# Kernel tuning notes

Measured on AMD Instinct MI355X. Metric: run time of the kernel, lower is better.

Reference implementation:

```python
import jax, jax.numpy as jnp
import numpy as np

N = 8192
PERCENT_ON = 0.1
K = int(round(N * PERCENT_ON))  # 819
BOOST_STRENGTH = 1.0


def setup_inputs() -> dict:
    key = jax.random.key(0)
    k1, k2 = jax.random.split(key)
    x = jax.random.normal(k1, (4096, N), dtype=jnp.float32)
    duty_cycles = jax.random.uniform(k2, (N,), dtype=jnp.float32) * 0.2
    return {"x": x, "duty_cycles": duty_cycles}


def reference(x, duty_cycles):
    # boost factors: exp((target_density - duty_cycle) * boost_strength)
    boost_strength = jnp.maximum(jnp.float32(BOOST_STRENGTH), 0.0)
    target_density = jnp.float32(K / N)
    boost_factors = jnp.exp((target_density - duty_cycles) * boost_strength)
    boosted = x * boost_factors  # [B, N]
    # top-k on boosted values, but transmit ORIGINAL x values at winning units
    _, idx = jax.lax.top_k(boosted, K)  # idx: [B, K]
    updates = jnp.take_along_axis(x, idx, axis=1)  # [B, K]
    rows = jnp.arange(x.shape[0])[:, None]  # [B, 1]
    out = jnp.zeros_like(x).at[rows, idx].set(updates)
    return out
```

## Files before the change

### kernel.cpp

```cpp
#include <hip/hip_runtime.h>
#include <math.h>

#define NCOL 8192
#define NROW 4096
#define KSEL 819
#define TPB  128
#define VPT  16
#define NBKT 1024
#define KPIV 0xBF866666u
#define LCAP 64

typedef float f32x4 __attribute__((ext_vector_type(4)));

__device__ __align__(16) float g_boost[NCOL];

__global__ void boost_kernel(const float* __restrict__ duty) {
    int i = blockIdx.x * blockDim.x + threadIdx.x;
    if (i < NCOL) {
        float diff = (0.0999755859375f - duty[i]);
        g_boost[i] = (float)exp((double)diff);
    }
}

__device__ __forceinline__ unsigned f2k(float f) {
    unsigned u = __float_as_uint(f);
    return u ^ (0x80000000u | (unsigned)((int)u >> 31));
}
__device__ __forceinline__ int kbucket(unsigned k) {
    int b = (int)(k >> 14) - (int)(KPIV >> 14);
    return (b > NBKT - 1) ? (NBKT - 1) : b;
}

__global__ __launch_bounds__(TPB) void kwinners_kernel(const float* __restrict__ x,
                                                       float* __restrict__ out) {
    __shared__ __align__(16) int hist[NBKT];
    __shared__ unsigned list[LCAP];
    __shared__ int wtot[2];
    __shared__ int lds_cnt, lds_sel, lds_R, lds_E;

    const int t = threadIdx.x, lane = t & 63, w = t >> 6;
    const int row = blockIdx.x;
    const f32x4* x4 = (const f32x4*)(x + (size_t)row * NCOL);
    const f32x4* b4 = (const f32x4*)g_boost;
    f32x4* o4 = (f32x4*)(out + (size_t)row * NCOL);

    unsigned kr[VPT][4];

    {
        const int4 z = make_int4(0, 0, 0, 0);
        ((int4*)hist)[2 * t] = z; ((int4*)hist)[2 * t + 1] = z;
        if (t == 0) lds_cnt = 0;
    }
#pragma unroll
    for (int j = 0; j < VPT; ++j) {
        f32x4 xx = x4[t + TPB * j];
        f32x4 bb = b4[t + TPB * j];
        kr[j][0] = f2k(xx.x * bb.x);
        kr[j][1] = f2k(xx.y * bb.y);
        kr[j][2] = f2k(xx.z * bb.z);
        kr[j][3] = f2k(xx.w * bb.w);
    }
    __syncthreads();

#pragma unroll
    for (int j = 0; j < VPT; ++j)
#pragma unroll
        for (int c = 0; c < 4; ++c) {
            unsigned k = kr[j][c];
            if (k > KPIV) atomicAdd(&hist[kbucket(k)], 1);
        }
    __syncthreads();

    int arr[16];
    {
        int4 a0 = ((const int4*)hist)[4 * lane + 0];
        int4 a1 = ((const int4*)hist)[4 * lane + 1];
        int4 a2 = ((const int4*)hist)[4 * lane + 2];
        int4 a3 = ((const int4*)hist)[4 * lane + 3];
        arr[0]=a0.x; arr[1]=a0.y; arr[2]=a0.z; arr[3]=a0.w;
        arr[4]=a1.x; arr[5]=a1.y; arr[6]=a1.z; arr[7]=a1.w;
        arr[8]=a2.x; arr[9]=a2.y; arr[10]=a2.z; arr[11]=a2.w;
        arr[12]=a3.x; arr[13]=a3.y; arr[14]=a3.z; arr[15]=a3.w;
    }
    int ts = 0;
#pragma unroll
    for (int b = 0; b < 16; ++b) ts += arr[b];
    int s = ts;
#pragma unroll
    for (int off = 1; off < 64; off <<= 1) {
        int o = __shfl_down(s, off);
        if (lane + off < 64) s += o;
    }
    const int C = __shfl(s, 0);

    unsigned th = 0; int Rf = 0, E = 0;
    bool fb = (C < KSEL);

    if (!fb) {
        const int S_ab = s - ts;
        bool cross = (S_ab < KSEL) && (S_ab + ts >= KSEL);
        int sel_l = 0, r1_l = 0;
        if (cross) {
            int cum = S_ab;
#pragma unroll
            for (int b = 15; b >= 0; --b) {
                int nx = cum + arr[b];
                if (cum < KSEL && nx >= KSEL) { sel_l = 16 * lane + b; r1_l = KSEL - cum; }
                cum = nx;
            }
        }
        unsigned long long m = __ballot(cross);
        int src = (int)__ffsll(m) - 1;
        const int sel = __shfl(sel_l, src);
        const int R1  = __shfl(r1_l, src);

#pragma unroll
        for (int j = 0; j < VPT; ++j)
#pragma unroll
            for (int c = 0; c < 4; ++c) {
                unsigned k = kr[j][c];
                if (k > KPIV && kbucket(k) == sel) {
                    int sl = atomicAdd(&lds_cnt, 1);
                    if (sl < LCAP) list[sl] = k;
                }
            }
        __syncthreads();
        const int n = lds_cnt;
        if (n > LCAP) fb = true;
        else {
            unsigned myk = (lane < n) ? list[lane] : 0u;
            int g = 0, e = 0;
            for (int i = 0; i < n; ++i) {
                unsigned ki = __shfl(myk, i);
                g += (ki > myk) ? 1 : 0;
                e += (ki == myk) ? 1 : 0;
            }
            unsigned cand = (lane < n && g < R1 && g + e >= R1) ? myk : 0u;
#pragma unroll
            for (int off = 1; off < 64; off <<= 1) {
                unsigned o = __shfl_xor(cand, off);
                cand = (o > cand) ? o : cand;
            }
            th = cand;

            int GE = 0;
#pragma unroll
            for (int j = 0; j < VPT; ++j) {
                f32x4 xx = x4[t + TPB * j];
                unsigned k0 = kr[j][0], k1 = kr[j][1], k2 = kr[j][2], k3 = kr[j][3];
                GE += (k0 > th) + (k1 > th) + (k2 > th) + (k3 > th);
                GE += ((k0 == th) + (k1 == th) + (k2 == th) + (k3 == th)) << 16;
                f32x4 rr;
                rr.x = (k0 >= th) ? xx.x : 0.0f;
                rr.y = (k1 >= th) ? xx.y : 0.0f;
                rr.z = (k2 >= th) ? xx.z : 0.0f;
                rr.w = (k3 >= th) ? xx.w : 0.0f;
                __builtin_nontemporal_store(rr, &o4[t + TPB * j]);
            }
#pragma unroll
            for (int off = 1; off < 64; off <<= 1) GE += __shfl_xor(GE, off);
            if (lane == 0) wtot[w] = GE;
            __syncthreads();
            const int GEt = wtot[0] + wtot[1];
            const int G = GEt & 0xFFFF, Eg = GEt >> 16;
            if (G < KSEL && G + Eg >= KSEL) { Rf = KSEL - G; E = Eg; }
            else fb = true;
        }
    }

    if (fb) {
        asm volatile("s_waitcnt vmcnt(0)" ::: "memory");
        __syncthreads();
        unsigned prefix = 0; int R = KSEL;
        for (int p = 0; p < 4; ++p) {
            const int sh = 24 - 8 * p;
            if (t < 64) ((int4*)hist)[t] = make_int4(0, 0, 0, 0);
            __syncthreads();
#pragma unroll
            for (int j = 0; j < VPT; ++j)
#pragma unroll
                for (int c = 0; c < 4; ++c) {
                    unsigned k = kr[j][c];
                    if (p == 0 || (k >> (sh + 8)) == (prefix >> (sh + 8)))
                        atomicAdd(&hist[(k >> sh) & 255u], 1);
                }
            __syncthreads();
            const int b0 = hist[2 * t], b1 = hist[2 * t + 1];
            int ts2 = b0 + b1, s2 = ts2;
#pragma unroll
            for (int off = 1; off < 64; off <<= 1) {
                int o = __shfl_down(s2, off);
                if (lane + off < 64) s2 += o;
            }
            if (lane == 0) wtot[w] = s2;
            __syncthreads();
            const int S_later = (w == 0) ? wtot[1] : 0;
            const int S_ab2 = (s2 - ts2) + S_later;
            if (S_ab2 < R && S_ab2 + ts2 >= R) {
                int cum = S_ab2;
                int nx = cum + b1;
                if (cum < R && nx >= R) { lds_sel = 2 * t + 1; lds_R = R - cum; lds_E = b1; }
                cum = nx; nx = cum + b0;
                if (cum < R && nx >= R) { lds_sel = 2 * t;     lds_R = R - cum; lds_E = b0; }
            }
            __syncthreads();
            prefix |= ((unsigned)lds_sel) << sh;
            R = lds_R;
        }
        th = prefix; Rf = R; E = lds_E;
#pragma unroll
        for (int j = 0; j < VPT; ++j) {
            f32x4 xx = x4[t + TPB * j];
            f32x4 rr;
            rr.x = (kr[j][0] >= th) ? xx.x : 0.0f;
            rr.y = (kr[j][1] >= th) ? xx.y : 0.0f;
            rr.z = (kr[j][2] >= th) ? xx.z : 0.0f;
            rr.w = (kr[j][3] >= th) ? xx.w : 0.0f;
            o4[t + TPB * j] = rr;
        }
    }

    if (E > Rf) {
        asm volatile("s_waitcnt vmcnt(0)" ::: "memory");
        __syncthreads();
        unsigned short* tl = (unsigned short*)hist;
        if (t == 0) lds_cnt = 0;
        __syncthreads();
#pragma unroll
        for (int j = 0; j < VPT; ++j)
#pragma unroll
            for (int c = 0; c < 4; ++c)
                if (kr[j][c] == th) {
                    int sl = atomicAdd(&lds_cnt, 1);
                    if (sl < 2048) tl[sl] = (unsigned short)(4 * (t + TPB * j) + c);
                }
        __syncthreads();
        const int ntie = lds_cnt;
        float* orow = out + (size_t)row * NCOL;
        if (ntie <= 2048) {
#pragma unroll
            for (int j = 0; j < VPT; ++j)
#pragma unroll
                for (int c = 0; c < 4; ++c)
                    if (kr[j][c] == th) {
                        const int col = 4 * (t + TPB * j) + c;
                        int rk = 0;
                        for (int i = 0; i < ntie; ++i) rk += (tl[i] < col) ? 1 : 0;
                        if (rk >= Rf) orow[col] = 0.0f;
                    }
        } else if (t == 0) {
            int seen = 0;
            for (int col = 0; col < NCOL; ++col) {
                float v = x[(size_t)row * NCOL + col] * g_boost[col];
                if (f2k(v) == th) { if (seen >= Rf) orow[col] = 0.0f; ++seen; }
            }
        }
    }
}

extern "C" void kernel_launch(void* const* d_in, const int* in_sizes, int n_in,
                              void* d_out, int out_size, void* d_ws, size_t ws_size,
                              hipStream_t stream) {
    const float* x = (const float*)d_in[0];
    const float* duty = (const float*)d_in[1];
    float* out = (float*)d_out;
    (void)in_sizes; (void)n_in; (void)out_size; (void)d_ws; (void)ws_size;

    boost_kernel<<<(NCOL + 255) / 256, 256, 0, stream>>>(duty);
    kwinners_kernel<<<NROW, TPB, 0, stream>>>(x, out);
}
```

Before: 73.59 us.

## Split k-winners into threshold and apply kernels with float-domain bucketing

Splits the fused kernel in two. The first kernel computes a per-row threshold, remainder and tie count and writes them to the workspace. A second kernel re-reads x and the boost factors, then writes the masked output. It also doubles threads per block, halves values per thread, and buckets on float values with a linear scale instead of key bits. The aim is to cut register pressure and raise occupancy, at the cost of reading x twice (an extra 128MB of traffic) plus an extra launch.

```diff
diff --git a/kernel.cpp b/kernel.cpp
--- a/kernel.cpp
+++ b/kernel.cpp
@@ -4,10 +4,11 @@
 #define NCOL 8192
 #define NROW 4096
 #define KSEL 819
-#define TPB  128
-#define VPT  16
+#define TPB  256
+#define VPT  8
 #define NBKT 1024
-#define KPIV 0xBF866666u
+#define PIV  1.05f
+#define BSCALE 512.0f
 #define LCAP 64
 
 typedef float f32x4 __attribute__((ext_vector_type(4)));
@@ -26,77 +27,83 @@
     unsigned u = __float_as_uint(f);
     return u ^ (0x80000000u | (unsigned)((int)u >> 31));
 }
-__device__ __forceinline__ int kbucket(unsigned k) {
-    int b = (int)(k >> 14) - (int)(KPIV >> 14);
+__device__ __forceinline__ float k2f(unsigned k) {
+    unsigned u = (k & 0x80000000u) ? (k ^ 0x80000000u) : ~k;
+    return __uint_as_float(u);
+}
+__device__ __forceinline__ int vbucket(float v) {
+    int b = (int)((v - PIV) * BSCALE);
+    b = (b < 0) ? 0 : b;
     return (b > NBKT - 1) ? (NBKT - 1) : b;
 }
 
-__global__ __launch_bounds__(TPB) void kwinners_kernel(const float* __restrict__ x,
-                                                       float* __restrict__ out) {
+__global__ __launch_bounds__(TPB) void thresh_kernel(const float* __restrict__ x,
+                                                     float* __restrict__ thf,
+                                                     int* __restrict__ rfo,
+                                                     int* __restrict__ eo) {
     __shared__ __align__(16) int hist[NBKT];
-    __shared__ unsigned list[LCAP];
-    __shared__ int wtot[2];
+    __shared__ float list[LCAP];
+    __shared__ int wtot[4];
     __shared__ int lds_cnt, lds_sel, lds_R, lds_E;
 
     const int t = threadIdx.x, lane = t & 63, w = t >> 6;
     const int row = blockIdx.x;
     const f32x4* x4 = (const f32x4*)(x + (size_t)row * NCOL);
     const f32x4* b4 = (const f32x4*)g_boost;
-    f32x4* o4 = (f32x4*)(out + (size_t)row * NCOL);
-
-    unsigned kr[VPT][4];
-
-    {
-        const int4 z = make_int4(0, 0, 0, 0);
-        ((int4*)hist)[2 * t] = z; ((int4*)hist)[2 * t + 1] = z;
-        if (t == 0) lds_cnt = 0;
-    }
+
+    f32x4 vv[VPT];
+
+    ((int4*)hist)[t] = make_int4(0, 0, 0, 0);
+    if (t == 0) lds_cnt = 0;
+
 #pragma unroll
     for (int j = 0; j < VPT; ++j) {
         f32x4 xx = x4[t + TPB * j];
         f32x4 bb = b4[t + TPB * j];
-        kr[j][0] = f2k(xx.x * bb.x);
-        kr[j][1] = f2k(xx.y * bb.y);
-        kr[j][2] = f2k(xx.z * bb.z);
-        kr[j][3] = f2k(xx.w * bb.w);
+        vv[j].x = xx.x * bb.x; vv[j].y = xx.y * bb.y;
+        vv[j].z = xx.z * bb.z; vv[j].w = xx.w * bb.w;
     }
     __syncthreads();
 
-#pragma unroll
-    for (int j = 0; j < VPT; ++j)
+    int cnt = 0;
+#pragma unroll
+    for (int j = 0; j < VPT; ++j) {
 #pragma unroll
         for (int c = 0; c < 4; ++c) {
-            unsigned k = kr[j][c];
-            if (k > KPIV) atomicAdd(&hist[kbucket(k)], 1);
-        }
+            float v = vv[j][c];
+            if (v > PIV) { ++cnt; atomicAdd(&hist[vbucket(v)], 1); }
+        }
+    }
+#pragma unroll
+    for (int off = 32; off; off >>= 1) cnt += __shfl_down(cnt, off);
+    if (lane == 0) wtot[w] = cnt;
     __syncthreads();
 
-    int arr[16];
-    {
-        int4 a0 = ((const int4*)hist)[4 * lane + 0];
-        int4 a1 = ((const int4*)hist)[4 * lane + 1];
-        int4 a2 = ((const int4*)hist)[4 * lane + 2];
-        int4 a3 = ((const int4*)hist)[4 * lane + 3];
-        arr[0]=a0.x; arr[1]=a0.y; arr[2]=a0.z; arr[3]=a0.w;
-        arr[4]=a1.x; arr[5]=a1.y; arr[6]=a1.z; arr[7]=a1.w;
-        arr[8]=a2.x; arr[9]=a2.y; arr[10]=a2.z; arr[11]=a2.w;
-        arr[12]=a3.x; arr[13]=a3.y; arr[14]=a3.z; arr[15]=a3.w;
-    }
-    int ts = 0;
-#pragma unroll
-    for (int b = 0; b < 16; ++b) ts += arr[b];
-    int s = ts;
-#pragma unroll
-    for (int off = 1; off < 64; off <<= 1) {
-        int o = __shfl_down(s, off);
-        if (lane + off < 64) s += o;
-    }
-    const int C = __shfl(s, 0);
-
-    unsigned th = 0; int Rf = 0, E = 0;
+    const int C = wtot[0] + wtot[1] + wtot[2] + wtot[3];
+    float th = 0.0f; int Rf = 0, E = 0;
     bool fb = (C < KSEL);
 
     if (!fb) {
+        int arr[16];
+        {
+            int4 a0 = ((const int4*)hist)[4 * lane + 0];
+            int4 a1 = ((const int4*)hist)[4 * lane + 1];
+            int4 a2 = ((const int4*)hist)[4 * lane + 2];
+            int4 a3 = ((const int4*)hist)[4 * lane + 3];
+            arr[0]=a0.x; arr[1]=a0.y; arr[2]=a0.z; arr[3]=a0.w;
+            arr[4]=a1.x; arr[5]=a1.y; arr[6]=a1.z; arr[7]=a1.w;
+            arr[8]=a2.x; arr[9]=a2.y; arr[10]=a2.z; arr[11]=a2.w;
+            arr[12]=a3.x; arr[13]=a3.y; arr[14]=a3.z; arr[15]=a3.w;
+        }
+        int ts = 0;
+#pragma unroll
+        for (int b = 0; b < 16; ++b) ts += arr[b];
+        int s = ts;
+#pragma unroll
+        for (int off = 1; off < 64; off <<= 1) {
+            int o = __shfl_down(s, off);
+            if (lane + off < 64) s += o;
+        }
         const int S_ab = s - ts;
         bool cross = (S_ab < KSEL) && (S_ab + ts >= KSEL);
         int sel_l = 0, r1_l = 0;
@@ -118,50 +125,42 @@
         for (int j = 0; j < VPT; ++j)
 #pragma unroll
             for (int c = 0; c < 4; ++c) {
-                unsigned k = kr[j][c];
-                if (k > KPIV && kbucket(k) == sel) {
+                float v = vv[j][c];
+                if (v > PIV && vbucket(v) == sel) {
                     int sl = atomicAdd(&lds_cnt, 1);
-                    if (sl < LCAP) list[sl] = k;
+                    if (sl < LCAP) list[sl] = v;
                 }
             }
         __syncthreads();
         const int n = lds_cnt;
-        if (n > LCAP) fb = true;
+        if (n > LCAP || n < 1) fb = true;
         else {
-            unsigned myk = (lane < n) ? list[lane] : 0u;
+            float myv = (lane < n) ? list[lane] : 0.0f;
             int g = 0, e = 0;
             for (int i = 0; i < n; ++i) {
-                unsigned ki = __shfl(myk, i);
-                g += (ki > myk) ? 1 : 0;
-                e += (ki == myk) ? 1 : 0;
-            }
-            unsigned cand = (lane < n && g < R1 && g + e >= R1) ? myk : 0u;
-#pragma unroll
-            for (int off = 1; off < 64; off <<= 1) {
-                unsigned o = __shfl_xor(cand, off);
-                cand = (o > cand) ? o : cand;
-            }
+                float vi = __shfl(myv, i);
+                g += (vi > myv) ? 1 : 0;
+                e += (vi == myv) ? 1 : 0;
+            }
+            float cand = (lane < n && g < R1 && g + e >= R1) ? myv : 0.0f;
+#pragma unroll
+            for (int off = 1; off < 64; off <<= 1)
+                cand = fmaxf(cand, __shfl_xor(cand, off));
             th = cand;
 
             int GE = 0;
 #pragma unroll
-            for (int j = 0; j < VPT; ++j) {
-                f32x4 xx = x4[t + TPB * j];
-                unsigned k0 = kr[j][0], k1 = kr[j][1], k2 = kr[j][2], k3 = kr[j][3];
-                GE += (k0 > th) + (k1 > th) + (k2 > th) + (k3 > th);
-                GE += ((k0 == th) + (k1 == th) + (k2 == th) + (k3 == th)) << 16;
-                f32x4 rr;
-                rr.x = (k0 >= th) ? xx.x : 0.0f;
-                rr.y = (k1 >= th) ? xx.y : 0.0f;
-                rr.z = (k2 >= th) ? xx.z : 0.0f;
-                rr.w = (k3 >= th) ? xx.w : 0.0f;
-                __builtin_nontemporal_store(rr, &o4[t + TPB * j]);
-            }
+            for (int j = 0; j < VPT; ++j)
+#pragma unroll
+                for (int c = 0; c < 4; ++c) {
+                    float v = vv[j][c];
+                    GE += (v > th ? 1 : 0) + (v == th ? (1 << 16) : 0);
+                }
 #pragma unroll
             for (int off = 1; off < 64; off <<= 1) GE += __shfl_xor(GE, off);
             if (lane == 0) wtot[w] = GE;
             __syncthreads();
-            const int GEt = wtot[0] + wtot[1];
+            const int GEt = wtot[0] + wtot[1] + wtot[2] + wtot[3];
             const int G = GEt & 0xFFFF, Eg = GEt >> 16;
             if (G < KSEL && G + Eg >= KSEL) { Rf = KSEL - G; E = Eg; }
             else fb = true;
@@ -169,24 +168,21 @@
     }
 
     if (fb) {
-        asm volatile("s_waitcnt vmcnt(0)" ::: "memory");
-        __syncthreads();
         unsigned prefix = 0; int R = KSEL;
         for (int p = 0; p < 4; ++p) {
             const int sh = 24 - 8 * p;
-            if (t < 64) ((int4*)hist)[t] = make_int4(0, 0, 0, 0);
+            hist[t] = 0;
             __syncthreads();
 #pragma unroll
             for (int j = 0; j < VPT; ++j)
 #pragma unroll
                 for (int c = 0; c < 4; ++c) {
-                    unsigned k = kr[j][c];
+                    unsigned k = f2k(vv[j][c]);
                     if (p == 0 || (k >> (sh + 8)) == (prefix >> (sh + 8)))
                         atomicAdd(&hist[(k >> sh) & 255u], 1);
                 }
             __syncthreads();
-            const int b0 = hist[2 * t], b1 = hist[2 * t + 1];
-            int ts2 = b0 + b1, s2 = ts2;
+            int h = hist[t], s2 = h;
 #pragma unroll
             for (int off = 1; off < 64; off <<= 1) {
                 int o = __shfl_down(s2, off);
@@ -194,65 +190,92 @@
             }
             if (lane == 0) wtot[w] = s2;
             __syncthreads();
-            const int S_later = (w == 0) ? wtot[1] : 0;
-            const int S_ab2 = (s2 - ts2) + S_later;
-            if (S_ab2 < R && S_ab2 + ts2 >= R) {
-                int cum = S_ab2;
-                int nx = cum + b1;
-                if (cum < R && nx >= R) { lds_sel = 2 * t + 1; lds_R = R - cum; lds_E = b1; }
-                cum = nx; nx = cum + b0;
-                if (cum < R && nx >= R) { lds_sel = 2 * t;     lds_R = R - cum; lds_E = b0; }
-            }
+            int S_later = 0;
+#pragma unroll
+            for (int w2 = 0; w2 < 4; ++w2) if (w2 > w) S_later += wtot[w2];
+            const int S_ab2 = (s2 - h) + S_later;
+            if (S_ab2 < R && S_ab2 + h >= R) { lds_sel = t; lds_R = R - S_ab2; lds_E = h; }
             __syncthreads();
             prefix |= ((unsigned)lds_sel) << sh;
             R = lds_R;
         }
-        th = prefix; Rf = R; E = lds_E;
+        th = k2f(prefix); Rf = R; E = lds_E;
+    }
+
+    if (t == 0) { thf[row] = th; rfo[row] = Rf; eo[row] = E; }
+}
+
+__global__ __launch_bounds__(TPB) void apply_kernel(const float* __restrict__ x,
+                                                    const float* __restrict__ thf,
+                                                    const int* __restrict__ rfo,
+                                                    const int* __restrict__ eo,
+                                                    float* __restrict__ out) {
+    __shared__ unsigned short tl[2048];
+    __shared__ int lds_cnt;
+
+    const int t = threadIdx.x;
+    const int row = blockIdx.x;
+    const f32x4* x4 = (const f32x4*)(x + (size_t)row * NCOL);
+    const f32x4* b4 = (const f32x4*)g_boost;
+    f32x4* o4 = (f32x4*)(out + (size_t)row * NCOL);
+
+    const float th = thf[row];
+    const int Rf = rfo[row], E = eo[row];
+
+#pragma unroll
+    for (int j = 0; j < VPT; ++j) {
+        f32x4 xx = x4[t + TPB * j];
+        f32x4 bb = b4[t + TPB * j];
+        f32x4 rr;
+        rr.x = (xx.x * bb.x >= th) ? xx.x : 0.0f;
+        rr.y = (xx.y * bb.y >= th) ? xx.y : 0.0f;
+        rr.z = (xx.z * bb.z >= th) ? xx.z : 0.0f;
+        rr.w = (xx.w * bb.w >= th) ? xx.w : 0.0f;
+        __builtin_nontemporal_store(rr, &o4[t + TPB * j]);
+    }
+
+    if (E > Rf) {
+        asm volatile("s_waitcnt vmcnt(0)" ::: "memory");
+        __syncthreads();
+        if (t == 0) lds_cnt = 0;
+        __syncthreads();
 #pragma unroll
         for (int j = 0; j < VPT; ++j) {
             f32x4 xx = x4[t + TPB * j];
-            f32x4 rr;
-            rr.x = (kr[j][0] >= th) ? xx.x : 0.0f;
-            rr.y = (kr[j][1] >= th) ? xx.y : 0.0f;
-            rr.z = (kr[j][2] >= th) ? xx.z : 0.0f;
-            rr.w = (kr[j][3] >= th) ? xx.w : 0.0f;
-            o4[t + TPB * j] = rr;
-        }
-    }
-
-    if (E > Rf) {
-        asm volatile("s_waitcnt vmcnt(0)" ::: "memory");
-        __syncthreads();
-        unsigned short* tl = (unsigned short*)hist;
-        if (t == 0) lds_cnt = 0;
-        __syncthreads();
-#pragma unroll
-        for (int j = 0; j < VPT; ++j)
-#pragma unroll
-            for (int c = 0; c < 4; ++c)
-                if (kr[j][c] == th) {
+            f32x4 bb = b4[t + TPB * j];
+#pragma unroll
+            for (int c = 0; c < 4; ++c) {
+                float v = xx[c] * bb[c];
+                if (v == th) {
                     int sl = atomicAdd(&lds_cnt, 1);
                     if (sl < 2048) tl[sl] = (unsigned short)(4 * (t + TPB * j) + c);
                 }
+            }
+        }
         __syncthreads();
         const int ntie = lds_cnt;
         float* orow = out + (size_t)row * NCOL;
         if (ntie <= 2048) {
 #pragma unroll
-            for (int j = 0; j < VPT; ++j)
-#pragma unroll
-                for (int c = 0; c < 4; ++c)
-                    if (kr[j][c] == th) {
+            for (int j = 0; j < VPT; ++j) {
+                f32x4 xx = x4[t + TPB * j];
+                f32x4 bb = b4[t + TPB * j];
+#pragma unroll
+                for (int c = 0; c < 4; ++c) {
+                    float v = xx[c] * bb[c];
+                    if (v == th) {
                         const int col = 4 * (t + TPB * j) + c;
                         int rk = 0;
                         for (int i = 0; i < ntie; ++i) rk += (tl[i] < col) ? 1 : 0;
                         if (rk >= Rf) orow[col] = 0.0f;
                     }
+                }
+            }
         } else if (t == 0) {
             int seen = 0;
             for (int col = 0; col < NCOL; ++col) {
                 float v = x[(size_t)row * NCOL + col] * g_boost[col];
-                if (f2k(v) == th) { if (seen >= Rf) orow[col] = 0.0f; ++seen; }
+                if (v == th) { if (seen >= Rf) orow[col] = 0.0f; ++seen; }
             }
         }
     }
@@ -264,8 +287,13 @@
     const float* x = (const float*)d_in[0];
     const float* duty = (const float*)d_in[1];
     float* out = (float*)d_out;
-    (void)in_sizes; (void)n_in; (void)out_size; (void)d_ws; (void)ws_size;
+    (void)in_sizes; (void)n_in; (void)out_size; (void)ws_size;
+
+    float* thf = (float*)d_ws;
+    int*   rfo = (int*)d_ws + NROW;
+    int*   eo  = (int*)d_ws + 2 * NROW;
 
     boost_kernel<<<(NCOL + 255) / 256, 256, 0, stream>>>(duty);
-    kwinners_kernel<<<NROW, TPB, 0, stream>>>(x, out);
-}
+    thresh_kernel<<<NROW, TPB, 0, stream>>>(x, thf, rfo, eo);
+    apply_kernel<<<NROW, TPB, 0, stream>>>(x, thf, rfo, eo, out);
+}
```

New measurement: 77.32 us. +5.1%, slower.
